# Performance work log

Measured on AMD Instinct MI355X. Metric: run time of the kernel, lower is better.

Reference implementation:

```python
import jax, jax.numpy as jnp
import numpy as np
from jax import lax

CURRICULUM_EP = 12
LI, LS, LW = 0.5, 0.8, 3.0


def _gauss_win(ws, C, dtype):
    coords = jnp.arange(ws, dtype=jnp.float32) - ws // 2
    g = jnp.exp(-coords ** 2 / (2 * 1.5 ** 2))
    win = g[None, :] * g[:, None]
    win = win / win.sum()
    # depthwise kernel, OIHW with I=1, O=C
    return jnp.broadcast_to(win[None, None], (C, 1, ws, ws)).astype(dtype)


def _dwconv(x, win, p, C):
    return lax.conv_general_dilated(
        x, win, window_strides=(1, 1), padding=[(p, p), (p, p)],
        dimension_numbers=('NCHW', 'OIHW', 'NCHW'), feature_group_count=C)


def diff_ssim(x, y, ws=11):
    C1, C2 = 0.01 ** 2, 0.03 ** 2
    C = x.shape[1]
    p = ws // 2
    win = _gauss_win(ws, C, x.dtype)
    mx = _dwconv(x, win, p, C)
    my = _dwconv(y, win, p, C)
    sxx = _dwconv(x * x, win, p, C) - mx ** 2
    syy = _dwconv(y * y, win, p, C) - my ** 2
    sxy = _dwconv(x * y, win, p, C) - mx * my
    ssim_map = (2 * mx * my + C1) * (2 * sxy + C2) / ((mx ** 2 + my ** 2 + C1) * (sxx + syy + C2))
    return ssim_map.mean()


def setup_inputs() -> dict:
    key = jax.random.key(0)
    k1, k2, k3, k4 = jax.random.split(key, 4)
    B, C, H, W = 16, 3, 512, 512
    NB = 1024  # watermark bits
    eps = 1e-4
    cover = jax.random.uniform(k1, (B, C, H, W), dtype=jnp.float32)
    wmed = jax.random.uniform(k2, (B, C, H, W), dtype=jnp.float32)
    wm_orig = jax.random.uniform(k3, (B, NB), dtype=jnp.float32)
    wm_ext = jnp.clip(jax.random.uniform(k4, (B, NB), dtype=jnp.float32), eps, 1.0 - eps)
    return {"cover": cover, "wmed": wmed, "wm_orig": wm_orig, "wm_ext": wm_ext, "epoch": 20}


def reference(cover, wmed, wm_orig, wm_ext, epoch):
    ml = jnp.mean((wmed - cover) ** 2)
    sv = diff_ssim(wmed, cover)
    sl = 1.0 - sv
    wl = jnp.mean(-(wm_orig * jnp.log(wm_ext) + (1.0 - wm_orig) * jnp.log(1.0 - wm_ext)))
    if epoch <= CURRICULUM_EP:
        w_img, w_ssim = 0.05, 0.05
    else:
        progress = min(1.0, (epoch - CURRICULUM_EP) / 10.0)
        w_img = 0.05 + (LI - 0.05) * progress
        w_ssim = 0.05 + (LS - 0.05) * progress
    total = w_img * ml + w_ssim * sl + LW * wl
    return (total, ml, sv, wl)
```

## Files before the change

kernel.cpp:

```cpp
#include <hip/hip_runtime.h>
#include <math.h>

#define H_IMG 512
#define W_IMG 512
#define TW 32
#define CH 32
#define NCHUNK 4
#define STRIP (CH*NCHUNK)
#define HALO 5
#define WS11 11
#define RING 42
#define RS 36
#define FSTR (RING*RS)
#define NF 4
#define NTHREADS 256

typedef float f2 __attribute__((ext_vector_type(2)));

__host__ __device__ constexpr float WT(int t) {
    return (t==0||t==10) ? 0.00102838f :
           (t==1||t==9)  ? 0.00759873f :
           (t==2||t==8)  ? 0.03600075f :
           (t==3||t==7)  ? 0.10936070f :
           (t==4||t==6)  ? 0.21300556f :
           (t==5)        ? 0.26601172f : 0.0f;
}

static __device__ __forceinline__ f2 splat2(float v) { f2 r = {v, v}; return r; }

__global__ __launch_bounds__(NTHREADS, 6) void ssim_mse_tile(
        const float* __restrict__ cover, const float* __restrict__ wmed,
        float* __restrict__ part, int nParts) {
    __shared__ __align__(16) float rbuf[NF*FSTR];

    const int tid = threadIdx.x;
    const int bx  = blockIdx.x & 15;
    const int ys  = (blockIdx.x >> 4) & 3;
    const int pl  = blockIdx.x >> 6;
    const size_t pbase = (size_t)pl * (H_IMG*W_IMG);
    const float* xp = wmed + pbase;
    const float* yp = cover + pbase;
    const int Y0  = ys << 7;
    const int tx0 = bx*TW - HALO;
    const bool xin = (bx != 0) && (bx != 15);

    float ssim_acc = 0.f, mse_acc = 0.f;

    for (int k = 0; k < NCHUNK; ++k) {
        const int nrows = (k == 0) ? (CH + 2*HALO) : CH;
        const int hr0   = (k == 0) ? -HALO : (CH*k + HALO);
        const int ntask = nrows << 3;

        for (int t = tid; t < ntask; t += NTHREADS) {
            const int r  = t >> 3, c0 = (t & 7) << 2;
            const int hr = hr0 + r;
            const int gy = Y0 + hr;
            const int slot = (hr + HALO) % RING;
            const bool rok = (unsigned)gy < (unsigned)H_IMG;
            float xv[14], yv[14];
            if (rok && xin) {
                const int ga = tx0 + c0 - 3;
                const float* rx = xp + (size_t)gy*W_IMG + ga;
                const float* ry = yp + (size_t)gy*W_IMG + ga;
                float4 XA = *(const float4*)(rx);
                float4 XB = *(const float4*)(rx + 4);
                float4 XC = *(const float4*)(rx + 8);
                float4 XD = *(const float4*)(rx + 12);
                float  XE = rx[16];
                float4 YA = *(const float4*)(ry);
                float4 YB = *(const float4*)(ry + 4);
                float4 YC = *(const float4*)(ry + 8);
                float4 YD = *(const float4*)(ry + 12);
                float  YE = ry[16];
                xv[0]=XA.w;  xv[1]=XB.x;  xv[2]=XB.y;  xv[3]=XB.z;  xv[4]=XB.w;
                xv[5]=XC.x;  xv[6]=XC.y;  xv[7]=XC.z;  xv[8]=XC.w;  xv[9]=XD.x;
                xv[10]=XD.y; xv[11]=XD.z; xv[12]=XD.w; xv[13]=XE;
                yv[0]=YA.w;  yv[1]=YB.x;  yv[2]=YB.y;  yv[3]=YB.z;  yv[4]=YB.w;
                yv[5]=YC.x;  yv[6]=YC.y;  yv[7]=YC.z;  yv[8]=YC.w;  yv[9]=YD.x;
                yv[10]=YD.y; yv[11]=YD.z; yv[12]=YD.w; yv[13]=YE;
            } else if (rok) {
                const int gc = tx0 + c0;
                const float* prx = xp + (size_t)gy*W_IMG + gc;
                const float* pry = yp + (size_t)gy*W_IMG + gc;
#pragma unroll
                for (int j = 0; j < 14; ++j) {
                    bool ok = (unsigned)(gc + j) < (unsigned)W_IMG;
                    xv[j] = ok ? prx[j] : 0.f;
                    yv[j] = ok ? pry[j] : 0.f;
                }
            } else {
#pragma unroll
                for (int j = 0; j < 14; ++j) { xv[j] = 0.f; yv[j] = 0.f; }
            }

            const bool own = (unsigned)hr < (unsigned)STRIP;

            f2 A[NF][2];
#pragma unroll
            for (int f = 0; f < NF; ++f) { A[f][0] = splat2(0.f); A[f][1] = splat2(0.f); }
#pragma unroll
            for (int j = 0; j < 14; ++j) {
                float sj = xv[j] + yv[j];
                float dj = xv[j] - yv[j];
                float s2 = sj*sj, d2 = dj*dj;
                if (j >= 5 && j < 9) {
                    if (own) mse_acc += d2;
                }
#pragma unroll
                for (int p = 0; p < 2; ++p) {
                    const int t0 = j - 2*p;
                    if (t0 >= 0 && t0 <= WS11) {
                        const f2 wp = {WT(t0), WT(t0-1)};
                        A[0][p] = __builtin_elementwise_fma(wp, splat2(sj), A[0][p]);
                        A[1][p] = __builtin_elementwise_fma(wp, splat2(dj), A[1][p]);
                        A[2][p] = __builtin_elementwise_fma(wp, splat2(s2), A[2][p]);
                        A[3][p] = __builtin_elementwise_fma(wp, splat2(d2), A[3][p]);
                    }
                }
            }
            float* wb = &rbuf[slot*RS + c0];
#pragma unroll
            for (int f = 0; f < NF; ++f) {
                *(float4*)(wb + f*FSTR) =
                    make_float4(A[f][0].x, A[f][0].y, A[f][1].x, A[f][1].y);
            }
        }
        __syncthreads();

        {
            const int c  = tid & 31;
            const int rg = tid >> 5;
            const int sb = (CH*k + (rg << 2)) % RING;
            f2 acc[NF][2];
#pragma unroll
            for (int f = 0; f < NF; ++f) {
                acc[f][0] = splat2(0.f); acc[f][1] = splat2(0.f);
            }
            const float* bp = rbuf + c;
#pragma unroll
            for (int i = 0; i < 14; ++i) {
                int sl = sb + i; if (sl >= RING) sl -= RING;
                const float* rp = bp + sl*RS;
#pragma unroll
                for (int f = 0; f < NF; ++f) {
                    float v = rp[f*FSTR];
#pragma unroll
                    for (int p = 0; p < 2; ++p) {
                        const int t0 = i - 2*p;
                        if (t0 >= 0 && t0 <= WS11) {
                            const f2 wp = {WT(t0), WT(t0-1)};
                            acc[f][p] = __builtin_elementwise_fma(wp, splat2(v), acc[f][p]);
                        }
                    }
                }
            }
            const f2 c1v = {1e-4f, 1e-4f};
            const f2 c2v = {9e-4f, 9e-4f};
            const f2 half = {0.5f, 0.5f};
#pragma unroll
            for (int p = 0; p < 2; ++p) {
                f2 S = acc[0][p], D = acc[1][p];
                f2 Cs = acc[2][p], Cd = acc[3][p];
                f2 SS = S*S, DD = D*D;
                f2 mxmy2 = (SS - DD) * half;
                f2 msq   = (SS + DD) * half;
                f2 sxy2  = (Cs - Cd) * half - mxmy2;
                f2 ssum  = (Cs + Cd) * half - msq;
                f2 num = (mxmy2 + c1v) * (sxy2 + c2v);
                f2 den = (msq + c1v) * (ssum + c2v);
                ssim_acc += __fdividef(num.x, den.x) + __fdividef(num.y, den.y);
            }
        }
        __syncthreads();
    }

#pragma unroll
    for (int off = 32; off > 0; off >>= 1) {
        ssim_acc += __shfl_down(ssim_acc, off);
        mse_acc  += __shfl_down(mse_acc, off);
    }
    const int wid = tid >> 6, lane = tid & 63;
    if (lane == 0) { rbuf[wid] = ssim_acc; rbuf[4+wid] = mse_acc; }
    __syncthreads();
    if (tid == 0) {
        part[blockIdx.x] = rbuf[0]+rbuf[1]+rbuf[2]+rbuf[3];
        part[nParts + blockIdx.x] = rbuf[4]+rbuf[5]+rbuf[6]+rbuf[7];
    }
}

#define FT 1024
__global__ __launch_bounds__(FT) void finalize_k(
        const float* __restrict__ part, int nParts,
        const float* __restrict__ wm_orig, const float* __restrict__ wm_ext,
        int nWm, const int* __restrict__ epoch_p,
        float* __restrict__ out, double inv_npix, double inv_nwm) {
    __shared__ double red[48];
    int tid = threadIdx.x;
    double s_ssim = 0.0, s_mse = 0.0, s_wl = 0.0;
    const float4* s4 = (const float4*)part;
    const float4* m4 = (const float4*)(part + nParts);
    int n4 = nParts >> 2;
    for (int i = tid; i < n4; i += FT) {
        float4 v = s4[i];
        s_ssim += (double)((v.x + v.y) + (v.z + v.w));
        float4 u = m4[i];
        s_mse  += (double)((u.x + u.y) + (u.z + u.w));
    }
    const float4* p4 = (const float4*)wm_orig;
    const float4* q4 = (const float4*)wm_ext;
    int w4 = nWm >> 2;
    for (int i = tid; i < w4; i += FT) {
        float4 p = p4[i], q = q4[i];
        float a;
        a  = -(p.x*__logf(q.x) + (1.f-p.x)*__logf(1.f-q.x));
        a += -(p.y*__logf(q.y) + (1.f-p.y)*__logf(1.f-q.y));
        a += -(p.z*__logf(q.z) + (1.f-p.z)*__logf(1.f-q.z));
        a += -(p.w*__logf(q.w) + (1.f-p.w)*__logf(1.f-q.w));
        s_wl += (double)a;
    }
#pragma unroll
    for (int off = 32; off > 0; off >>= 1) {
        s_ssim += __shfl_down(s_ssim, off);
        s_mse  += __shfl_down(s_mse, off);
        s_wl   += __shfl_down(s_wl, off);
    }
    int wid = tid >> 6, lane = tid & 63;
    if (lane == 0) { red[wid] = s_ssim; red[16+wid] = s_mse; red[32+wid] = s_wl; }
    __syncthreads();
    if (tid == 0) {
        double ssim_sum = 0.0, mse_sum = 0.0, wl_sum = 0.0;
        for (int i = 0; i < 16; ++i) {
            ssim_sum += red[i]; mse_sum += red[16+i]; wl_sum += red[32+i];
        }
        float sv = (float)(ssim_sum * inv_npix);
        float ml = (float)(mse_sum  * inv_npix);
        float wl = (float)(wl_sum   * inv_nwm);
        int e = *epoch_p;
        float w_img, w_ssim;
        if (e <= 12) {
            w_img = 0.05f; w_ssim = 0.05f;
        } else {
            float progress = fminf(1.0f, (float)(e - 12) / 10.0f);
            w_img  = 0.05f + (0.5f - 0.05f)*progress;
            w_ssim = 0.05f + (0.8f - 0.05f)*progress;
        }
        float sl = 1.0f - sv;
        float total = w_img*ml + w_ssim*sl + 3.0f*wl;
        out[0] = total;
        out[1] = ml;
        out[2] = sv;
        out[3] = wl;
    }
}

extern "C" void kernel_launch(void* const* d_in, const int* in_sizes, int n_in,
                              void* d_out, int out_size, void* d_ws, size_t ws_size,
                              hipStream_t stream) {
    const float* cover   = (const float*)d_in[0];
    const float* wmed    = (const float*)d_in[1];
    const float* wm_orig = (const float*)d_in[2];
    const float* wm_ext  = (const float*)d_in[3];
    const int*   epoch   = (const int*)d_in[4];
    float* out = (float*)d_out;

    int npix   = in_sizes[0];
    int planes = npix / (H_IMG * W_IMG);
    int nWm    = in_sizes[2];

    int nBlocks = 16 * 4 * planes;
    int nParts  = nBlocks;
    float* part = (float*)d_ws;

    ssim_mse_tile<<<nBlocks, NTHREADS, 0, stream>>>(cover, wmed, part, nParts);
    finalize_k<<<1, FT, 0, stream>>>(part, nParts, wm_orig, wm_ext, nWm,
                                     epoch, out,
                                     1.0 / (double)npix, 1.0 / (double)nWm);
}
```

Before: 174.7 us.

## Double strip height and block size, vectorize edge-column loads

Each block now covers a 256-row strip in 64-row chunks with 512 threads, halving the block count and the fraction of rows re-read as vertical halo. The shared ring buffer grows to fit the taller chunks, and the reduction is widened to eight waves. Edge blocks now use predicated float4 loads instead of a scalar per-element path. The larger LDS footprint and block size lower the number of resident blocks per CU and reduce how many blocks there are to spread across the CUs.

```diff
diff --git a/kernel.cpp b/kernel.cpp
--- a/kernel.cpp
+++ b/kernel.cpp
@@ -4,16 +4,16 @@
 #define H_IMG 512
 #define W_IMG 512
 #define TW 32
-#define CH 32
+#define CH 64
 #define NCHUNK 4
 #define STRIP (CH*NCHUNK)
 #define HALO 5
 #define WS11 11
-#define RING 42
+#define RING 74
 #define RS 36
 #define FSTR (RING*RS)
 #define NF 4
-#define NTHREADS 256
+#define NTHREADS 512
 
 typedef float f2 __attribute__((ext_vector_type(2)));
 
@@ -28,19 +28,19 @@
 
 static __device__ __forceinline__ f2 splat2(float v) { f2 r = {v, v}; return r; }
 
-__global__ __launch_bounds__(NTHREADS, 6) void ssim_mse_tile(
+__global__ __launch_bounds__(NTHREADS, 4) void ssim_mse_tile(
         const float* __restrict__ cover, const float* __restrict__ wmed,
         float* __restrict__ part, int nParts) {
     __shared__ __align__(16) float rbuf[NF*FSTR];
 
     const int tid = threadIdx.x;
     const int bx  = blockIdx.x & 15;
-    const int ys  = (blockIdx.x >> 4) & 3;
-    const int pl  = blockIdx.x >> 6;
+    const int ys  = (blockIdx.x >> 4) & 1;
+    const int pl  = blockIdx.x >> 5;
     const size_t pbase = (size_t)pl * (H_IMG*W_IMG);
     const float* xp = wmed + pbase;
     const float* yp = cover + pbase;
-    const int Y0  = ys << 7;
+    const int Y0  = ys << 8;
     const int tx0 = bx*TW - HALO;
     const bool xin = (bx != 0) && (bx != 15);
 
@@ -58,36 +58,47 @@
             const int slot = (hr + HALO) % RING;
             const bool rok = (unsigned)gy < (unsigned)H_IMG;
             float xv[14], yv[14];
-            if (rok && xin) {
+            if (rok) {
                 const int ga = tx0 + c0 - 3;
                 const float* rx = xp + (size_t)gy*W_IMG + ga;
                 const float* ry = yp + (size_t)gy*W_IMG + ga;
-                float4 XA = *(const float4*)(rx);
-                float4 XB = *(const float4*)(rx + 4);
-                float4 XC = *(const float4*)(rx + 8);
-                float4 XD = *(const float4*)(rx + 12);
-                float  XE = rx[16];
-                float4 YA = *(const float4*)(ry);
-                float4 YB = *(const float4*)(ry + 4);
-                float4 YC = *(const float4*)(ry + 8);
-                float4 YD = *(const float4*)(ry + 12);
-                float  YE = ry[16];
+                float4 XA, XB, XC, XD, YA, YB, YC, YD;
+                float  XE, YE;
+                if (xin) {
+                    XA = *(const float4*)(rx);
+                    XB = *(const float4*)(rx + 4);
+                    XC = *(const float4*)(rx + 8);
+                    XD = *(const float4*)(rx + 12);
+                    XE = rx[16];
+                    YA = *(const float4*)(ry);
+                    YB = *(const float4*)(ry + 4);
+                    YC = *(const float4*)(ry + 8);
+                    YD = *(const float4*)(ry + 12);
+                    YE = ry[16];
+                } else {
+                    const float4 z4 = make_float4(0.f, 0.f, 0.f, 0.f);
+                    const bool okA = (unsigned)(ga     ) <= (unsigned)(W_IMG-4);
+                    const bool okB = (unsigned)(ga +  4) <= (unsigned)(W_IMG-4);
+                    const bool okC = (unsigned)(ga +  8) <= (unsigned)(W_IMG-4);
+                    const bool okD = (unsigned)(ga + 12) <= (unsigned)(W_IMG-4);
+                    const bool okE = (unsigned)(ga + 16) <= (unsigned)(W_IMG-1);
+                    XA = okA ? *(const float4*)(rx)      : z4;
+                    XB = okB ? *(const float4*)(rx + 4)  : z4;
+                    XC = okC ? *(const float4*)(rx + 8)  : z4;
+                    XD = okD ? *(const float4*)(rx + 12) : z4;
+                    XE = okE ? rx[16] : 0.f;
+                    YA = okA ? *(const float4*)(ry)      : z4;
+                    YB = okB ? *(const float4*)(ry + 4)  : z4;
+                    YC = okC ? *(const float4*)(ry + 8)  : z4;
+                    YD = okD ? *(const float4*)(ry + 12) : z4;
+                    YE = okE ? ry[16] : 0.f;
+                }
                 xv[0]=XA.w;  xv[1]=XB.x;  xv[2]=XB.y;  xv[3]=XB.z;  xv[4]=XB.w;
                 xv[5]=XC.x;  xv[6]=XC.y;  xv[7]=XC.z;  xv[8]=XC.w;  xv[9]=XD.x;
                 xv[10]=XD.y; xv[11]=XD.z; xv[12]=XD.w; xv[13]=XE;
                 yv[0]=YA.w;  yv[1]=YB.x;  yv[2]=YB.y;  yv[3]=YB.z;  yv[4]=YB.w;
                 yv[5]=YC.x;  yv[6]=YC.y;  yv[7]=YC.z;  yv[8]=YC.w;  yv[9]=YD.x;
                 yv[10]=YD.y; yv[11]=YD.z; yv[12]=YD.w; yv[13]=YE;
-            } else if (rok) {
-                const int gc = tx0 + c0;
-                const float* prx = xp + (size_t)gy*W_IMG + gc;
-                const float* pry = yp + (size_t)gy*W_IMG + gc;
-#pragma unroll
-                for (int j = 0; j < 14; ++j) {
-                    bool ok = (unsigned)(gc + j) < (unsigned)W_IMG;
-                    xv[j] = ok ? prx[j] : 0.f;
-                    yv[j] = ok ? pry[j] : 0.f;
-                }
             } else {
 #pragma unroll
                 for (int j = 0; j < 14; ++j) { xv[j] = 0.f; yv[j] = 0.f; }
@@ -180,11 +191,14 @@
         mse_acc  += __shfl_down(mse_acc, off);
     }
     const int wid = tid >> 6, lane = tid & 63;
-    if (lane == 0) { rbuf[wid] = ssim_acc; rbuf[4+wid] = mse_acc; }
+    if (lane == 0) { rbuf[wid] = ssim_acc; rbuf[8+wid] = mse_acc; }
     __syncthreads();
     if (tid == 0) {
-        part[blockIdx.x] = rbuf[0]+rbuf[1]+rbuf[2]+rbuf[3];
-        part[nParts + blockIdx.x] = rbuf[4]+rbuf[5]+rbuf[6]+rbuf[7];
+        float s = 0.f, m = 0.f;
+#pragma unroll
+        for (int i = 0; i < 8; ++i) { s += rbuf[i]; m += rbuf[8+i]; }
+        part[blockIdx.x] = s;
+        part[nParts + blockIdx.x] = m;
     }
 }
 
@@ -267,7 +281,7 @@
     int planes = npix / (H_IMG * W_IMG);
     int nWm    = in_sizes[2];
 
-    int nBlocks = 16 * 4 * planes;
+    int nBlocks = 16 * 2 * planes;
     int nParts  = nBlocks;
     float* part = (float*)d_ws;
 
```

After: 174.6 us. No clear change (-0.1%).
